# Kernel tuning notes

Hardware: AMD Instinct MI355X
Metric: run time of the kernel (lower is better)

The kernel has to match this reference:

```python
import jax, jax.numpy as jnp
import numpy as np

EMBED_DIM = 1024
NUM_HEADS = 16
HEAD_DIM = EMBED_DIM // NUM_HEADS
ROPE_BASE = 10000.0


def rotate_half(x):
    d = x.shape[-1] // 2
    x1, x2 = x[..., :d], x[..., d:]
    return jnp.concatenate((-x2, x1), axis=-1)


def setup_inputs() -> dict:
    key = jax.random.key(0)
    k_x, k_wqkv, k_bqkv, k_wo, k_bo = jax.random.split(key, 5)
    C = EMBED_DIM
    x = jax.random.normal(k_x, (4, 2048, C), dtype=jnp.float32)
    s = 1.0 / np.sqrt(C)
    W_qkv = jax.random.uniform(k_wqkv, (C, 3 * C), minval=-s, maxval=s, dtype=jnp.float32)
    b_qkv = jax.random.uniform(k_bqkv, (3 * C,), minval=-s, maxval=s, dtype=jnp.float32)
    W_out = jax.random.uniform(k_wo, (C, C), minval=-s, maxval=s, dtype=jnp.float32)
    b_out = jax.random.uniform(k_bo, (C,), minval=-s, maxval=s, dtype=jnp.float32)
    return {"x": x, "W_qkv": W_qkv, "b_qkv": b_qkv, "W_out": W_out, "b_out": b_out}


def reference(x, W_qkv, b_qkv, W_out, b_out):
    B, T, C = x.shape
    H, Dh = NUM_HEADS, HEAD_DIM
    # fused QKV projection: [B,T,3C] -> [3,B,H,T,Dh]
    qkv = (x @ W_qkv + b_qkv).reshape(B, T, 3, H, Dh).transpose(2, 0, 3, 1, 4)
    q, k, v = qkv[0], qkv[1], qkv[2]
    # rotary embedding: freqs [T, Dh/2] -> emb [T, Dh]
    inv_freq = 1.0 / (ROPE_BASE ** (jnp.arange(0, Dh, 2, dtype=jnp.float32) / Dh))
    freqs = jnp.arange(T, dtype=jnp.float32)[:, None] * inv_freq[None, :]
    emb = jnp.concatenate((freqs, freqs), axis=-1)  # [T, Dh], broadcasts over B,H
    cos, sin = jnp.cos(emb), jnp.sin(emb)
    q = q * cos + rotate_half(q) * sin
    k = k * cos + rotate_half(k) * sin
    # full (non-causal) attention, manual softmax
    scale = 1.0 / np.sqrt(Dh)
    attn = jax.nn.softmax(jnp.einsum("bhqd,bhkd->bhqk", q, k) * scale, axis=-1)
    out = jnp.einsum("bhqk,bhkd->bhqd", attn, v)  # [B,H,T,Dh]
    out = out.transpose(0, 2, 1, 3).reshape(B, T, C)
    return out @ W_out + b_out
```

## Files before the change

kernel.cpp:

```cpp
#include <hip/hip_runtime.h>
#include <math.h>

#define T_SEQ 2048
#define CDIM  1024
#define NH    16
#define DHD   64
#define BATCH 4
#define MROWS (BATCH * T_SEQ)
#define BHN   (BATCH * NH)

typedef _Float16 f16;
typedef __attribute__((ext_vector_type(8))) _Float16 f16x8;
typedef __attribute__((ext_vector_type(4))) _Float16 f16x4;
typedef __attribute__((ext_vector_type(2))) _Float16 f16x2;
typedef __attribute__((ext_vector_type(2))) __fp16 fp16x2;
typedef __attribute__((ext_vector_type(4))) float f32x4;
typedef __attribute__((ext_vector_type(16))) float f32x16;
typedef __attribute__((ext_vector_type(4))) unsigned int uint4v;

__device__ __forceinline__ float fast_exp2(float x) {
#if __has_builtin(__builtin_amdgcn_exp2f)
    return __builtin_amdgcn_exp2f(x);
#else
    return exp2f(x);
#endif
}

__device__ __forceinline__ float fast_rcp(float x) {
#if __has_builtin(__builtin_amdgcn_rcpf)
    return __builtin_amdgcn_rcpf(x);
#else
    return 1.0f / x;
#endif
}

__device__ __forceinline__ f16x2 cvt_pk_f16(float a, float b) {
    fp16x2 r = __builtin_amdgcn_cvt_pkrtz(a, b);
    return __builtin_bit_cast(f16x2, r);
}

__device__ __forceinline__ void permlane32_swap(unsigned &a, unsigned &b) {
    asm volatile("v_permlane32_swap_b32 %0, %1" : "+v"(a), "+v"(b));
}

__device__ __forceinline__ void gl_lds16(const f16* g, f16* l) {
    __builtin_amdgcn_global_load_lds(
        (const __attribute__((address_space(1))) void*)(g),
        (__attribute__((address_space(3))) void*)(l),
        16, 0, 0);
}

__global__ __launch_bounds__(256) void prep_kernel(
    const float* __restrict__ X, f16* __restrict__ Xf,
    const float* __restrict__ Wq, const float* __restrict__ Wo,
    f16* __restrict__ Wqt, f16* __restrict__ Wot,
    float* __restrict__ ctab, float* __restrict__ stab)
{
    const int bx = blockIdx.x;
    if (bx < 256) {
        int idx = bx * 256 + threadIdx.x;
        int t = idx >> 5, i = idx & 31;
        double inv = pow(10000.0, -(double)(2 * i) / 64.0);
        double a = (double)t * inv;
        ctab[idx] = (float)cos(a);
        stab[idx] = (float)sin(a);
    } else if (bx < 4352) {
        int idx = (bx - 256) * 256 + threadIdx.x;
        const float4* src = (const float4*)X + (size_t)idx * 2;
        float4 a = src[0], b = src[1];
        f16x8 o;
        o[0] = (f16)a.x; o[1] = (f16)a.y; o[2] = (f16)a.z; o[3] = (f16)a.w;
        o[4] = (f16)b.x; o[5] = (f16)b.y; o[6] = (f16)b.z; o[7] = (f16)b.w;
        *((f16x8*)Xf + idx) = o;
    } else {
        const int sub = threadIdx.x >> 6, lane = threadIdx.x & 63;
        const int id = (bx - 4352) * 4 + sub;
        const int k0 = (id & 127) * 8;
        const int ny = id >> 7;
        const float* W;
        f16* Wt;
        int N, n;
        if (ny < 48) { W = Wq; Wt = Wqt; N = 3072; n = ny * 64 + lane; }
        else         { W = Wo; Wt = Wot; N = 1024; n = (ny - 48) * 64 + lane; }
        f16x8 o;
#pragma unroll
        for (int j = 0; j < 8; j++) o[j] = (f16)W[(size_t)(k0 + j) * N + n];
        *(f16x8*)(Wt + (size_t)n * CDIM + k0) = o;
    }
}

#define GEMM_MAINLOOP(Aimg, Bimg, M0, N0)                                         \
    __shared__ f16 As[128][64], Bs[128][64];                                      \
    const int tid = threadIdx.x, wave = tid >> 6, lane = tid & 63;                \
    const int l16 = lane & 15, quad = lane >> 4;                                  \
    const int wm = wave >> 1, wn = wave & 1;                                      \
    f32x4 acc[4][4];                                                              \
    _Pragma("unroll") for (int i = 0; i < 4; i++)                                 \
        _Pragma("unroll") for (int j = 0; j < 4; j++)                             \
            acc[i][j] = (f32x4){0.f, 0.f, 0.f, 0.f};                              \
    const f16* sbase = (wave < 2) ? (Aimg) : (Bimg);                              \
    f16* lbase = ((wave < 2) ? &As[0][0] : &Bs[0][0]) + (wave & 1) * 4096;        \
    const size_t srow0 = ((wave < 2) ? (size_t)(M0) : (size_t)(N0)) + (wave & 1) * 64; \
    const int srow = lane >> 3, schunk = lane & 7;                                \
    const int gchunk = (schunk ^ srow) << 3;         \
    for (int k0 = 0; k0 < CDIM; k0 += 64) {                                       \
        _Pragma("unroll") for (int it = 0; it < 8; it++)                          \
            gl_lds16(sbase + (srow0 + it * 8 + srow) * CDIM + k0 + gchunk,        \
                     lbase + it * 512);                                           \
        __syncthreads();                                                          \
        _Pragma("unroll") for (int ks = 0; ks < 2; ks++) {                        \
            f16x8 fa[4], fb[4];                                                   \
            _Pragma("unroll") for (int mi = 0; mi < 4; mi++)                      \
                fa[mi] = *(const f16x8*)                                          \
                    &As[wm * 64 + mi * 16 + l16][((ks * 4 + quad) ^ (l16 & 7)) << 3]; \
            _Pragma("unroll") for (int ni = 0; ni < 4; ni++)                      \
                fb[ni] = *(const f16x8*)                                          \
                    &Bs[wn * 64 + ni * 16 + l16][((ks * 4 + quad) ^ (l16 & 7)) << 3]; \
            _Pragma("unroll") for (int mi = 0; mi < 4; mi++)                      \
                _Pragma("unroll") for (int ni = 0; ni < 4; ni++)                  \
                    acc[mi][ni] = __builtin_amdgcn_mfma_f32_16x16x32_f16(         \
                        fa[mi], fb[ni], acc[mi][ni], 0, 0, 0);                    \
        }                                                                         \
        __syncthreads();                                                          \
    }

__global__ __launch_bounds__(256) void qkv_gemm_kernel(
    const f16* __restrict__ Xf, const f16* __restrict__ Wt,
    const float* __restrict__ bias,
    const float* __restrict__ ctab, const float* __restrict__ stab,
    f16* __restrict__ qf, f16* __restrict__ kf, f16* __restrict__ vtb)
{
    const int m0 = blockIdx.x * 128;
    const int n0 = blockIdx.y * 128;
    GEMM_MAINLOOP(Xf, Wt, m0, n0)

    const int ncol0 = n0 + wn * 64;
    const int w = ncol0 >> 10;
    const int h = (ncol0 >> 6) & 15;
    const int b = m0 >> 11;
    const int trow0 = (m0 & 2047) + wm * 64 + quad * 4;
    float bia[4];
#pragma unroll
    for (int ni = 0; ni < 4; ni++) bia[ni] = bias[ncol0 + ni * 16 + l16];

    if (w < 2) {
        f16* oq = w ? kf : qf;
        const float sc = w ? 1.0f : 0.18033688011112042f;
#pragma unroll
        for (int mi = 0; mi < 4; mi++) {
#pragma unroll
            for (int i = 0; i < 4; i++) {
                int t = trow0 + mi * 16 + i;
                size_t rowoff = ((size_t)(b * NH + h) * T_SEQ + t) * DHD;
#pragma unroll
                for (int np = 0; np < 2; np++) {
                    int d = np * 16 + l16;
                    float v0 = acc[mi][np][i] + bia[np];
                    float v1 = acc[mi][np + 2][i] + bia[np + 2];
                    float c = ctab[(t << 5) + d];
                    float s = stab[(t << 5) + d];
                    f16x2 pr;
                    pr[0] = (f16)((v0 * c - v1 * s) * sc);
                    pr[1] = (f16)((v1 * c + v0 * s) * sc);
                    *(f16x2*)(oq + rowoff + 2 * d) = pr;
                }
            }
        }
    } else {
#pragma unroll
        for (int mi = 0; mi < 4; mi++) {
            const int tb = trow0 + mi * 16;
#pragma unroll
            for (int ni = 0; ni < 4; ni++) {
                const int d = ni * 16 + l16;
                f16x4 pv;
#pragma unroll
                for (int i = 0; i < 4; i++) pv[i] = (f16)(acc[mi][ni][i] + bia[ni]);
                *(f16x4*)(vtb + ((size_t)(b * NH + h) * DHD + d) * T_SEQ + tb) = pv;
            }
        }
    }
}

__global__ __launch_bounds__(256, 4) void attn_kernel(
    const f16* __restrict__ qf, const f16* __restrict__ kf,
    const f16* __restrict__ vt, f16* __restrict__ ab)
{
    __shared__ f16 Kb[2][64][64];
    __shared__ f16 Vb[2][64][64];
    __shared__ float Lb[4][32];

    const int tid  = threadIdx.x;
    const int wave = tid >> 6, lane = tid & 63;
    const int l31  = lane & 31, hh = lane >> 5;

    const int flat = blockIdx.x + (blockIdx.y << 4);
    const int swz  = (flat & 7) * 128 + (flat >> 3);
    const int qt = swz & 15;
    const int bh = swz >> 4;
    const int q0 = qt * 128 + wave * 32;

    const f16* kbase = kf + (size_t)bh * T_SEQ * DHD;
    const f16* vbase = vt + (size_t)bh * DHD * T_SEQ;

    f16x8 qfr[4];
    {
        const f16* qrow = qf + ((size_t)bh * T_SEQ + q0 + l31) * DHD + hh * 8;
#pragma unroll
        for (int kk = 0; kk < 4; kk++)
            qfr[kk] = *(const f16x8*)(qrow + kk * 16);
    }

    f32x16 o[2];
#pragma unroll
    for (int db = 0; db < 2; db++)
#pragma unroll
        for (int r = 0; r < 16; r++) o[db][r] = 0.f;
    float lacc = 0.f;

    f32x16 zero16;
#pragma unroll
    for (int r = 0; r < 16; r++) zero16[r] = 0.f;

    const int srow = tid >> 3;
    const int schunk = tid & 7;
    const int gcol = (schunk ^ (srow & 7)) << 3;

    const f16* kg = kbase + (size_t)srow * DHD + gcol;
    const f16* vg = vbase + (size_t)srow * T_SEQ + gcol;

    {
        f16* kl = &Kb[0][wave * 8][0];
        f16* vl = &Vb[0][wave * 8][0];
        gl_lds16(kg, kl);
        gl_lds16(kg + 32 * DHD, kl + 32 * 64);
        gl_lds16(vg, vl);
        gl_lds16(vg + (size_t)32 * T_SEQ, vl + 32 * 64);
        kg += 64 * DHD;
        vg += 64;
    }
    __syncthreads();

    for (int kt = 0; kt < 32; kt++) {
        const int buf = kt & 1;
        if (kt < 31) {
            f16* kl = &Kb[buf ^ 1][wave * 8][0];
            f16* vl = &Vb[buf ^ 1][wave * 8][0];
            gl_lds16(kg, kl);
            gl_lds16(kg + 32 * DHD, kl + 32 * 64);
            gl_lds16(vg, vl);
            gl_lds16(vg + (size_t)32 * T_SEQ, vl + 32 * 64);
            kg += 64 * DHD;
            vg += 64;
        }

        f16x8 pA[4];
#pragma unroll
        for (int b2 = 0; b2 < 2; b2++) {
            f32x16 scc;
            __builtin_amdgcn_s_setprio(1);
#pragma unroll
            for (int kk = 0; kk < 4; kk++) {
                const int kc = ((kk * 2 + hh) ^ (l31 & 7)) << 3;
                f16x8 kfr = *(const f16x8*)&Kb[buf][b2 * 32 + l31][kc];
                scc = __builtin_amdgcn_mfma_f32_32x32x16_f16(
                    kfr, qfr[kk], kk == 0 ? zero16 : scc, 0, 0, 0);
            }
            __builtin_amdgcn_s_setprio(0);
            float e[16];
#pragma unroll
            for (int r = 0; r < 16; r++) {
                e[r] = fast_exp2(scc[r]);
                lacc += e[r];
            }
            unsigned pk[8];
#pragma unroll
            for (int i = 0; i < 8; i++)
                pk[i] = __builtin_bit_cast(unsigned,
                                           cvt_pk_f16(e[2 * i], e[2 * i + 1]));
            permlane32_swap(pk[0], pk[2]);
            permlane32_swap(pk[1], pk[3]);
            permlane32_swap(pk[4], pk[6]);
            permlane32_swap(pk[5], pk[7]);
            uint4v a0 = {pk[0], pk[1], pk[2], pk[3]};
            uint4v a1 = {pk[4], pk[5], pk[6], pk[7]};
            pA[b2 * 2]     = __builtin_bit_cast(f16x8, a0);
            pA[b2 * 2 + 1] = __builtin_bit_cast(f16x8, a1);
        }
        __builtin_amdgcn_s_setprio(1);
#pragma unroll
        for (int db = 0; db < 2; db++) {
#pragma unroll
            for (int kk = 0; kk < 4; kk++) {
                const int vc = ((kk * 2 + hh) ^ (l31 & 7)) << 3;
                f16x8 vfr = *(const f16x8*)&Vb[buf][db * 32 + l31][vc];
                o[db] = __builtin_amdgcn_mfma_f32_32x32x16_f16(
                    pA[kk], vfr, o[db], 0, 0, 0);
            }
        }
        __builtin_amdgcn_s_setprio(0);

        if (kt < 31) __syncthreads();
    }

    lacc += __shfl_xor(lacc, 32);
    if (lane < 32) Lb[wave][l31] = lacc;
    __syncthreads();
    f32x4 ivv[4];
#pragma unroll
    for (int g = 0; g < 4; g++)
        ivv[g] = *(const f32x4*)&Lb[wave][g * 8 + hh * 4];

    const int b = bh >> 4, h = bh & 15;
#pragma unroll
    for (int r = 0; r < 16; r++) {
        const int qrow = (r & 3) + 8 * (r >> 2) + 4 * hh;
        const int m = b * T_SEQ + qt * 128 + wave * 32 + qrow;
        const float iv = fast_rcp(ivv[r >> 2][r & 3]);
        f16* dst = ab + (size_t)m * CDIM + h * 64 + l31;
        dst[0]  = (f16)(o[0][r] * iv);
        dst[32] = (f16)(o[1][r] * iv);
    }
}

__global__ __launch_bounds__(256) void out_gemm_kernel(
    const f16* __restrict__ Ab, const f16* __restrict__ Wt,
    const float* __restrict__ bias, float* __restrict__ out)
{
    const int m0 = blockIdx.x * 128;
    const int n0 = blockIdx.y * 128;
    GEMM_MAINLOOP(Ab, Wt, m0, n0)

    const int ncol0 = n0 + wn * 64;
    float bia[4];
#pragma unroll
    for (int ni = 0; ni < 4; ni++) bia[ni] = bias[ncol0 + ni * 16 + l16];
#pragma unroll
    for (int mi = 0; mi < 4; mi++) {
#pragma unroll
        for (int i = 0; i < 4; i++) {
            int m = m0 + wm * 64 + mi * 16 + quad * 4 + i;
#pragma unroll
            for (int ni = 0; ni < 4; ni++)
                out[(size_t)m * CDIM + ncol0 + ni * 16 + l16] = acc[mi][ni][i] + bia[ni];
        }
    }
}

extern "C" void kernel_launch(void* const* d_in, const int* in_sizes, int n_in,
                              void* d_out, int out_size, void* d_ws, size_t ws_size,
                              hipStream_t stream)
{
    const float* x    = (const float*)d_in[0];
    const float* Wqkv = (const float*)d_in[1];
    const float* bqkv = (const float*)d_in[2];
    const float* Wout = (const float*)d_in[3];
    const float* bout = (const float*)d_in[4];
    float* out = (float*)d_out;

    const size_t XSZ  = (size_t)MROWS * CDIM;
    const size_t WQSZ = (size_t)3072 * CDIM;
    const size_t WOSZ = (size_t)CDIM * CDIM;
    const size_t QSZ  = (size_t)BHN * T_SEQ * DHD;

    char* p = (char*)d_ws;
    f16* Xf  = (f16*)p; p += XSZ * 2;
    f16* Wqt = (f16*)p; p += WQSZ * 2;
    f16* Wot = (f16*)p; p += WOSZ * 2;
    f16* qf  = (f16*)p; p += QSZ * 2;
    f16* kf  = (f16*)p; p += QSZ * 2;
    f16* vtb = (f16*)p; p += QSZ * 2;
    f16* ab  = (f16*)p; p += QSZ * 2;
    float* ctab = (float*)p; p += T_SEQ * 32 * 4;
    float* stab = (float*)p; p += T_SEQ * 32 * 4;

    prep_kernel<<<6400, 256, 0, stream>>>(x, Xf, Wqkv, Wout, Wqt, Wot, ctab, stab);
    qkv_gemm_kernel<<<dim3(64, 24), 256, 0, stream>>>(
        Xf, Wqt, bqkv, ctab, stab, qf, kf, vtb);
    attn_kernel<<<dim3(16, BHN), 256, 0, stream>>>(qf, kf, vtb, ab);
    out_gemm_kernel<<<dim3(64, 8), 256, 0, stream>>>(ab, Wot, bout, out);
}
```

Before: 280.7 us.

## Compute softmax row sums via MFMA and swizzle GEMM block order

```diff
diff --git a/kernel.cpp b/kernel.cpp
--- a/kernel.cpp
+++ b/kernel.cpp
@@ -130,8 +130,10 @@
     const float* __restrict__ ctab, const float* __restrict__ stab,
     f16* __restrict__ qf, f16* __restrict__ kf, f16* __restrict__ vtb)
 {
-    const int m0 = blockIdx.x * 128;
-    const int n0 = blockIdx.y * 128;
+    const int flat = blockIdx.x + (blockIdx.y << 6);
+    const int idx  = flat >> 3;
+    const int m0 = ((flat & 7) * 8 + (idx & 7)) * 128;
+    const int n0 = (idx >> 3) * 128;
     GEMM_MAINLOOP(Xf, Wt, m0, n0)
 
     const int ncol0 = n0 + wn * 64;
@@ -188,7 +190,6 @@
 {
     __shared__ f16 Kb[2][64][64];
     __shared__ f16 Vb[2][64][64];
-    __shared__ float Lb[4][32];
 
     const int tid  = threadIdx.x;
     const int wave = tid >> 6, lane = tid & 63;
@@ -216,11 +217,17 @@
     for (int db = 0; db < 2; db++)
 #pragma unroll
         for (int r = 0; r < 16; r++) o[db][r] = 0.f;
-    float lacc = 0.f;
+    f32x16 lacc16;
+#pragma unroll
+    for (int r = 0; r < 16; r++) lacc16[r] = 0.f;
 
     f32x16 zero16;
 #pragma unroll
     for (int r = 0; r < 16; r++) zero16[r] = 0.f;
+
+    f16x8 ones;
+#pragma unroll
+    for (int j = 0; j < 8; j++) ones[j] = (f16)1.0f;
 
     const int srow = tid >> 3;
     const int schunk = tid & 7;
@@ -269,10 +276,7 @@
             __builtin_amdgcn_s_setprio(0);
             float e[16];
 #pragma unroll
-            for (int r = 0; r < 16; r++) {
-                e[r] = fast_exp2(scc[r]);
-                lacc += e[r];
-            }
+            for (int r = 0; r < 16; r++) e[r] = fast_exp2(scc[r]);
             unsigned pk[8];
 #pragma unroll
             for (int i = 0; i < 8; i++)
@@ -289,6 +293,10 @@
         }
         __builtin_amdgcn_s_setprio(1);
 #pragma unroll
+        for (int kk = 0; kk < 4; kk++)
+            lacc16 = __builtin_amdgcn_mfma_f32_32x32x16_f16(
+                pA[kk], ones, lacc16, 0, 0, 0);
+#pragma unroll
         for (int db = 0; db < 2; db++) {
 #pragma unroll
             for (int kk = 0; kk < 4; kk++) {
@@ -303,20 +311,12 @@
         if (kt < 31) __syncthreads();
     }
 
-    lacc += __shfl_xor(lacc, 32);
-    if (lane < 32) Lb[wave][l31] = lacc;
-    __syncthreads();
-    f32x4 ivv[4];
-#pragma unroll
-    for (int g = 0; g < 4; g++)
-        ivv[g] = *(const f32x4*)&Lb[wave][g * 8 + hh * 4];
-
     const int b = bh >> 4, h = bh & 15;
 #pragma unroll
     for (int r = 0; r < 16; r++) {
         const int qrow = (r & 3) + 8 * (r >> 2) + 4 * hh;
         const int m = b * T_SEQ + qt * 128 + wave * 32 + qrow;
-        const float iv = fast_rcp(ivv[r >> 2][r & 3]);
+        const float iv = fast_rcp(lacc16[r]);
         f16* dst = ab + (size_t)m * CDIM + h * 64 + l31;
         dst[0]  = (f16)(o[0][r] * iv);
         dst[32] = (f16)(o[1][r] * iv);
@@ -327,8 +327,10 @@
     const f16* __restrict__ Ab, const f16* __restrict__ Wt,
     const float* __restrict__ bias, float* __restrict__ out)
 {
-    const int m0 = blockIdx.x * 128;
-    const int n0 = blockIdx.y * 128;
+    const int flat = blockIdx.x + (blockIdx.y << 6);
+    const int idx  = flat >> 3;
+    const int m0 = ((flat & 7) * 8 + (idx & 7)) * 128;
+    const int n0 = (idx >> 3) * 128;
     GEMM_MAINLOOP(Ab, Wt, m0, n0)
 
     const int ncol0 = n0 + wn * 64;
```

Result: no change. 282.4 us (+0.6%).
